# Kernel optimization log

Measured on AMD Instinct MI355X. Metric: run time of the kernel, lower is better.

The kernel has to match this reference:

```python
import jax, jax.numpy as jnp
import numpy as np
import math

N = 50000      # nodes
E = 600000     # edges per relation
R = 3          # relations (graph.etypes)
IN = 256       # in_feats
H = 128        # h_feats
D_ORDER = 2    # Bernstein order d -> d+1 thetas, each of length d+1


def _bernstein_thetas(d):
    # Coefficients (ascending powers) of (x/2)^i (1-x/2)^(d-i) / Beta(i+1, d+1-i)
    thetas = []
    for i in range(d + 1):
        a = np.zeros(i + 1); a[i] = 0.5 ** i                      # (x/2)^i
        b = np.array([math.comb(d - i, j) * (-0.5) ** j for j in range(d - i + 1)])  # (1-x/2)^(d-i)
        scale = math.factorial(d + 1) / (math.factorial(i) * math.factorial(d - i))  # 1/Beta
        thetas.append((np.convolve(a, b) * scale).astype(np.float32))
    return np.stack(thetas)  # [d+1, d+1]

THETAS = jnp.asarray(_bernstein_thetas(D_ORDER))  # [3, 3]


def _leaky(x):
    return jax.nn.leaky_relu(x, 0.01)


def _poly_feats(h, src, dst, n, k):
    # Laplacian power features T_0..T_{k-1}: T_0 = h, T_{j+1} = T_j - Dinv * A^T (Dinv * T_j)
    deg = jax.ops.segment_sum(jnp.ones_like(dst, dtype=h.dtype), dst, num_segments=n)
    dinv = jnp.clip(deg, 1.0) ** -0.5
    dinv = dinv[:, None]  # [N,1]
    feats = [h]
    f = h
    for _ in range(k - 1):
        agg = jax.ops.segment_sum((f * dinv)[src], dst, num_segments=n)  # copy_u + sum
        f = f - agg * dinv
        feats.append(f)
    return jnp.stack(feats)  # [k, N, H]


def setup_inputs() -> dict:
    key = jax.random.key(0)
    ks = jax.random.split(key, 32)
    inp = {"x": jax.random.normal(ks[0], (N, IN), dtype=jnp.float32)}
    for r in range(R):
        inp[f"src{r}"] = jax.random.randint(ks[1 + 2 * r], (E,), 0, N)
        inp[f"dst{r}"] = jax.random.randint(ks[2 + 2 * r], (E,), 0, N)
        inp[f"W1_{r}"] = jax.random.normal(ks[8 + 4 * r], (IN, H), dtype=jnp.float32) * 0.02
        inp[f"b1_{r}"] = jnp.zeros((H,), dtype=jnp.float32)
        inp[f"W2_{r}"] = jax.random.normal(ks[9 + 4 * r], (H, H), dtype=jnp.float32) * 0.02
        inp[f"b2_{r}"] = jnp.zeros((H,), dtype=jnp.float32)
    inp["W3"] = jax.random.normal(ks[30], (H * (D_ORDER + 1), H), dtype=jnp.float32) * 0.02
    inp["b3"] = jnp.zeros((H,), dtype=jnp.float32)
    return inp


def reference(x, src0, dst0, src1, dst1, src2, dst2,
              W1_0, b1_0, W2_0, b2_0,
              W1_1, b1_1, W2_1, b2_1,
              W1_2, b1_2, W2_2, b2_2,
              W3, b3):
    edges = [(src0, dst0), (src1, dst1), (src2, dst2)]
    params = [(W1_0, b1_0, W2_0, b2_0), (W1_1, b1_1, W2_1, b2_1), (W1_2, b1_2, W2_2, b2_2)]
    k = D_ORDER + 1
    acc = jnp.zeros((N, H), dtype=x.dtype)
    for (src, dst), (W1, b1, W2, b2) in zip(edges, params):
        h = _leaky(x @ W1 + b1)
        h = _leaky(h @ W2 + b2)            # dropout is identity in eval
        T = _poly_feats(h, src, dst, N, k)  # [k, N, H]
        # each PolyConv output j: sum_k theta[j,k] * T_k, concatenated over j
        hs = jnp.einsum('jk,knh->jnh', THETAS, T)          # [k, N, H]
        h_final = hs.transpose(1, 0, 2).reshape(N, k * H)   # concat along feature dim
        acc = acc + (h_final @ W3 + b3)
    return _leaky(acc)
```

## Files before the change

kernel.cpp:

```cpp
#include <hip/hip_runtime.h>
#include <hip/hip_bf16.h>

#define HDIM 128
#define TB_LD 1152
#define BCAP 8192
#define NBUCK 256

typedef __attribute__((ext_vector_type(8))) short short8;
typedef __attribute__((ext_vector_type(16))) float floatx16;

#define GF_LEAKY 1
#define GF_BF16  4

__global__ __launch_bounds__(256) void gemm_lds_kernel(
    const __hip_bfloat16* __restrict__ A, int lda, int aOff,
    const __hip_bfloat16* __restrict__ Bt, int ldb, int bRowOff,
    const float* __restrict__ bias, int biasOff,
    void* __restrict__ Cout, int ldc, int cColOff,
    int M, int K, int flags)
{
    __shared__ short As[128 * 64];
    __shared__ short Bs[128 * 64];

    const int tid  = threadIdx.x;
    const int lane = tid & 63;
    const int wave = tid >> 6;
    const int wm   = (wave >> 1) << 6;
    const int wn   = (wave & 1) << 6;
    const int l31  = lane & 31;
    const int ch   = lane >> 5;
    const int e7   = l31 & 7;

    const int m0 = blockIdx.x * 128;
    const int y  = blockIdx.y;

    const short* Ab = (const short*)A + (size_t)y * aOff;
    const short* Bb = (const short*)Bt + (size_t)y * bRowOff * ldb;

    const int rr = tid >> 3;
    const int cc = tid & 7;
    const int sbase = rr * 64 + (((cc ^ (rr & 7)) << 3));
    const short* pA[4];
    const short* pB[4];
#pragma unroll
    for (int i = 0; i < 4; i++) {
        int r = i * 32 + rr;
        int gr = m0 + r; gr = gr < M ? gr : (M - 1);
        pA[i] = Ab + (size_t)gr * lda + cc * 8;
        pB[i] = Bb + (size_t)r * ldb + cc * 8;
    }

    floatx16 acc[2][2];
#pragma unroll
    for (int a = 0; a < 2; a++)
#pragma unroll
        for (int b = 0; b < 2; b++)
#pragma unroll
            for (int i = 0; i < 16; i++) acc[a][b][i] = 0.f;

    const int ra0 = (wm + l31) * 64;
    const int ra1 = (wm + 32 + l31) * 64;
    const int rb0 = (wn + l31) * 64;
    const int rb1 = (wn + 32 + l31) * 64;

    for (int k0 = 0; k0 < K; k0 += 64) {
#pragma unroll
        for (int i = 0; i < 4; i++) {
            int4 av = *(const int4*)(pA[i] + k0);
            int4 bv = *(const int4*)(pB[i] + k0);
            *(int4*)(As + i * 2048 + sbase) = av;
            *(int4*)(Bs + i * 2048 + sbase) = bv;
        }
        __syncthreads();
#pragma unroll
        for (int ks = 0; ks < 4; ks++) {
            const int sw = (((ks << 1) + ch) ^ e7) << 3;
            short8 a0 = *(const short8*)(As + ra0 + sw);
            short8 a1 = *(const short8*)(As + ra1 + sw);
            short8 b0 = *(const short8*)(Bs + rb0 + sw);
            short8 b1 = *(const short8*)(Bs + rb1 + sw);
            acc[0][0] = __builtin_amdgcn_mfma_f32_32x32x16_bf16(a0, b0, acc[0][0], 0, 0, 0);
            acc[0][1] = __builtin_amdgcn_mfma_f32_32x32x16_bf16(a0, b1, acc[0][1], 0, 0, 0);
            acc[1][0] = __builtin_amdgcn_mfma_f32_32x32x16_bf16(a1, b0, acc[1][0], 0, 0, 0);
            acc[1][1] = __builtin_amdgcn_mfma_f32_32x32x16_bf16(a1, b1, acc[1][1], 0, 0, 0);
        }
        __syncthreads();
    }

    const int colL0 = wn + l31;
    const int ccol  = y * cColOff;
    const float bv0 = bias ? bias[y * biasOff + colL0] : 0.f;
    const float bv1 = bias ? bias[y * biasOff + colL0 + 32] : 0.f;
    const int rb = m0 + wm + ((lane >> 5) << 2);

#pragma unroll
    for (int tm = 0; tm < 2; tm++) {
#pragma unroll
        for (int rg = 0; rg < 16; rg++) {
            int row = rb + tm * 32 + (rg & 3) + ((rg >> 2) << 3);
            if (row >= M) continue;
            float v0 = acc[tm][0][rg] + bv0;
            float v1 = acc[tm][1][rg] + bv1;
            if (flags & GF_LEAKY) {
                v0 = v0 > 0.f ? v0 : 0.01f * v0;
                v1 = v1 > 0.f ? v1 : 0.01f * v1;
            }
            if (flags & GF_BF16) {
                __hip_bfloat16* C = (__hip_bfloat16*)Cout;
                C[(size_t)row * ldc + ccol + colL0]      = __float2bfloat16(v0);
                C[(size_t)row * ldc + ccol + colL0 + 32] = __float2bfloat16(v1);
            } else {
                float* C = (float*)Cout;
                C[(size_t)row * ldc + ccol + colL0]      = v0;
                C[(size_t)row * ldc + ccol + colL0 + 32] = v1;
            }
        }
    }
}

__global__ __launch_bounds__(256) void cvt_x_kernel(const float* __restrict__ in,
                                                    __hip_bfloat16* __restrict__ out,
                                                    int n4)
{
    int i = blockIdx.x * 256 + threadIdx.x;
    if (i >= n4) return;
    float4 v = *(const float4*)(in + (size_t)i * 4);
    __hip_bfloat16 o[4] = {__float2bfloat16(v.x), __float2bfloat16(v.y),
                           __float2bfloat16(v.z), __float2bfloat16(v.w)};
    *(uint2*)(out + (size_t)i * 4) = *(uint2*)o;
}

__global__ __launch_bounds__(256) void prep_weights_kernel(
    const float* __restrict__ W1_0, const float* __restrict__ W1_1, const float* __restrict__ W1_2,
    const float* __restrict__ W2_0, const float* __restrict__ W2_1, const float* __restrict__ W2_2,
    const float* __restrict__ W3,
    const float* __restrict__ b1_0, const float* __restrict__ b1_1, const float* __restrict__ b1_2,
    const float* __restrict__ b2_0, const float* __restrict__ b2_1, const float* __restrict__ b2_2,
    __hip_bfloat16* __restrict__ W1t, __hip_bfloat16* __restrict__ W2t,
    __hip_bfloat16* __restrict__ W3et, float* __restrict__ b1c, float* __restrict__ b2c)
{
    int idx = blockIdx.x * 256 + threadIdx.x;
    if (idx < 98304) {
        int r = idx >> 15, rem = idx & 32767;
        int k = rem >> 7, n = rem & 127;
        const float* W = (r == 0) ? W1_0 : (r == 1) ? W1_1 : W1_2;
        W1t[(size_t)(r * 128 + n) * 256 + k] = __float2bfloat16(W[rem]);
    } else if (idx < 147456) {
        int j = idx - 98304;
        int r = j >> 14, rem = j & 16383;
        int k = rem >> 7, n = rem & 127;
        const float* W = (r == 0) ? W2_0 : (r == 1) ? W2_1 : W2_2;
        W2t[(size_t)r * 16384 + n * 128 + k] = __float2bfloat16(W[rem]);
    } else if (idx < 196608) {
        int j = idx - 147456;
        int row = j >> 7, c = j & 127;
        int kk = row >> 7, hh = row & 127;
        const float t[3][3] = {{3.f, -3.f, 0.75f},
                               {0.f,  3.f, -1.5f},
                               {0.f,  0.f, 0.75f}};
        float s = 0.f;
        for (int jj = 0; jj < 3; jj++)
            s += t[jj][kk] * W3[((size_t)jj * HDIM + hh) * HDIM + c];
        __hip_bfloat16 sb = __float2bfloat16(s);
        W3et[(size_t)c * TB_LD + row]       = sb;
        W3et[(size_t)c * TB_LD + 384 + row] = sb;
        W3et[(size_t)c * TB_LD + 768 + row] = sb;
    } else if (idx < 196992) {
        int j = idx - 196608;
        const float* b = (j < 128) ? b1_0 : (j < 256) ? b1_1 : b1_2;
        b1c[j] = b[j & 127];
    } else if (idx < 197376) {
        int j = idx - 196992;
        const float* b = (j < 128) ? b2_0 : (j < 256) ? b2_1 : b2_2;
        b2c[j] = b[j & 127];
    }
}

__global__ __launch_bounds__(256) void bin_kernel(
    const int* __restrict__ s0, const int* __restrict__ s1, const int* __restrict__ s2,
    const int* __restrict__ d0, const int* __restrict__ d1, const int* __restrict__ d2,
    int* __restrict__ bcur,
    int* __restrict__ binned,
    int nE)
{
    __shared__ int hist[NBUCK];
    __shared__ int claim[NBUCK];
    const int t = threadIdx.x;
    const int y = blockIdx.y;
    const int* sp = (y == 0) ? s0 : (y == 1) ? s1 : s2;
    const int* dp = (y == 0) ? d0 : (y == 1) ? d1 : d2;
    const int base = blockIdx.x * 4096;

    hist[t] = 0;
    __syncthreads();

    int pk[16], bk[16], rk[16];
#pragma unroll
    for (int j = 0; j < 16; j++) {
        int e = base + j * 256 + t;
        if (e < nE) {
            int s = sp[e], d = dp[e];
            bk[j] = d >> 8;
            pk[j] = s | ((d & 255) << 16);
            rk[j] = atomicAdd(&hist[bk[j]], 1);
        } else {
            bk[j] = -1;
        }
    }
    __syncthreads();
    int cnt = hist[t];
    claim[t] = (cnt > 0) ? atomicAdd(&bcur[y * NBUCK + t], cnt) : 0;
    __syncthreads();
#pragma unroll
    for (int j = 0; j < 16; j++) {
        if (bk[j] >= 0) {
            int pos = claim[bk[j]] + rk[j];
            if (pos < BCAP)
                binned[((size_t)(y * NBUCK + bk[j])) * BCAP + pos] = pk[j];
        }
    }
}

__global__ __launch_bounds__(256) void deg_kernel2(
    const int* __restrict__ bcur, const int* __restrict__ binned,
    int* __restrict__ degi, float* __restrict__ dinvAll, int N)
{
    __shared__ int hist[256];
    const int t = threadIdx.x;
    const int b = blockIdx.x;
    const int y = blockIdx.y;
    hist[t] = 0;
    __syncthreads();
    const int count = bcur[y * NBUCK + b];
    const int* eb = binned + ((size_t)(y * NBUCK + b)) * BCAP;
    for (int i = t; i < count; i += 256)
        atomicAdd(&hist[(eb[i] >> 16) & 255], 1);
    __syncthreads();
    int node = (b << 8) + t;
    if (node < N) {
        int dg = hist[t];
        degi[(size_t)y * N + node] = dg;
        float d = dg > 1 ? (float)dg : 1.0f;
        dinvAll[(size_t)y * N + node] = 1.0f / sqrtf(d);
    }
}

__global__ __launch_bounds__(256) void place_kernel2(
    const int* __restrict__ bcur, const int* __restrict__ binned,
    const int* __restrict__ rowstart, int* __restrict__ ebuf, int N, int nE)
{
    __shared__ int cur[256];
    const int t = threadIdx.x;
    const int b = blockIdx.x;
    const int y = blockIdx.y;
    int node = (b << 8) + t;
    cur[t] = rowstart[(size_t)y * (N + 1) + (node < N ? node : N)];
    __syncthreads();
    const int count = bcur[y * NBUCK + b];
    const int* eb = binned + ((size_t)(y * NBUCK + b)) * BCAP;
    int* ebo = ebuf + (size_t)y * nE;
    for (int i = t; i < count; i += 256) {
        int p = eb[i];
        int pos = atomicAdd(&cur[(p >> 16) & 255], 1);
        ebo[pos] = p & 0xFFFF;
    }
}

__global__ __launch_bounds__(256) void scan_local_kernel(
    const int* __restrict__ degi, int* __restrict__ rowstart,
    int* __restrict__ bsum, int n)
{
    __shared__ int sdata[256];
    const int y = blockIdx.y;
    const int* in = degi + (size_t)y * n;
    int* out = rowstart + (size_t)y * (n + 1);
    int* bs  = bsum + y * 256;
    const int base = blockIdx.x * 1024;
    const int t = threadIdx.x;
    int v[4];
#pragma unroll
    for (int j = 0; j < 4; j++) {
        int idx = base + t * 4 + j;
        v[j] = (idx < n) ? in[idx] : 0;
    }
    int tsum = v[0] + v[1] + v[2] + v[3];
    sdata[t] = tsum;
    __syncthreads();
    for (int off = 1; off < 256; off <<= 1) {
        int x = (t >= off) ? sdata[t - off] : 0;
        __syncthreads();
        sdata[t] += x;
        __syncthreads();
    }
    int run = sdata[t] - tsum;
    if (t == 255) bs[blockIdx.x] = sdata[255];
#pragma unroll
    for (int j = 0; j < 4; j++) {
        int idx = base + t * 4 + j;
        if (idx < n) out[idx] = run;
        run += v[j];
    }
}

__global__ __launch_bounds__(256) void scan_bsum_kernel(int* __restrict__ bsum, int nB)
{
    __shared__ int sdata[256];
    int* bs = bsum + blockIdx.y * 256;
    const int t = threadIdx.x;
    int val = (t < nB) ? bs[t] : 0;
    sdata[t] = val;
    __syncthreads();
    for (int off = 1; off < 256; off <<= 1) {
        int x = (t >= off) ? sdata[t - off] : 0;
        __syncthreads();
        sdata[t] += x;
        __syncthreads();
    }
    if (t < nB) bs[t] = sdata[t] - val;
}

__global__ __launch_bounds__(256) void scan_add_kernel(
    int* __restrict__ rowstart, const int* __restrict__ bsum, int n, int nE)
{
    int i = blockIdx.x * 256 + threadIdx.x;
    int y = blockIdx.y;
    int* rs = rowstart + (size_t)y * (n + 1);
    const int* bs = bsum + y * 256;
    if (i < n) {
        rs[i] = rs[i] + bs[i >> 10];
    } else if (i == n) {
        rs[n] = nE;
    }
}

__device__ inline float bflo(unsigned u) {
    return __builtin_bit_cast(float, u << 16);
}
__device__ inline float bfhi(unsigned u) {
    return __builtin_bit_cast(float, u & 0xffff0000u);
}

__device__ inline void acc8(float* s, uint4 u, float w) {
    s[0] += bflo(u.x) * w; s[1] += bfhi(u.x) * w;
    s[2] += bflo(u.y) * w; s[3] += bfhi(u.y) * w;
    s[4] += bflo(u.z) * w; s[5] += bfhi(u.z) * w;
    s[6] += bflo(u.w) * w; s[7] += bfhi(u.w) * w;
}

__global__ __launch_bounds__(256) void gather_agg_kernel(
    const int* __restrict__ rowstart, const int* __restrict__ ebufAll,
    const float* __restrict__ dinvAll, __hip_bfloat16* __restrict__ T,
    int inBase, int outBase, int N, int nE)
{
    int v = blockIdx.x * 16 + (threadIdx.x >> 4);
    if (v >= N) return;
    const int y = blockIdx.y;
    const int* rs = rowstart + (size_t)y * (N + 1);
    const int* eb = ebufAll + (size_t)y * nE;
    const float* dinv = dinvAll + (size_t)y * N;
    const int inOff  = y * 384 + inBase;
    const int outOff = y * 384 + outBase;

    const int lane8 = (threadIdx.x & 15) << 3;
    const unsigned short* Tu = (const unsigned short*)T;
    const int beg = rs[v];
    const int end = rs[v + 1];

    float s[8];
#pragma unroll
    for (int j = 0; j < 8; j++) s[j] = 0.f;

    int i = beg;
    for (; i + 3 < end; i += 4) {
        int a = eb[i], b = eb[i + 1], c = eb[i + 2], d = eb[i + 3];
        float wa = dinv[a], wb = dinv[b], wc = dinv[c], wd = dinv[d];
        uint4 ua = *(const uint4*)(Tu + (size_t)a * TB_LD + inOff + lane8);
        uint4 ub = *(const uint4*)(Tu + (size_t)b * TB_LD + inOff + lane8);
        uint4 uc = *(const uint4*)(Tu + (size_t)c * TB_LD + inOff + lane8);
        uint4 ud = *(const uint4*)(Tu + (size_t)d * TB_LD + inOff + lane8);
        acc8(s, ua, wa); acc8(s, ub, wb); acc8(s, uc, wc); acc8(s, ud, wd);
    }
    for (; i < end; i++) {
        int a = eb[i];
        float wa = dinv[a];
        uint4 ua = *(const uint4*)(Tu + (size_t)a * TB_LD + inOff + lane8);
        acc8(s, ua, wa);
    }

    const float di = dinv[v];
    uint4 uv = *(const uint4*)(Tu + (size_t)v * TB_LD + inOff + lane8);
    float r[8] = {bflo(uv.x) - s[0] * di, bfhi(uv.x) - s[1] * di,
                  bflo(uv.y) - s[2] * di, bfhi(uv.y) - s[3] * di,
                  bflo(uv.z) - s[4] * di, bfhi(uv.z) - s[5] * di,
                  bflo(uv.w) - s[6] * di, bfhi(uv.w) - s[7] * di};
    __hip_bfloat16 o[8];
#pragma unroll
    for (int j = 0; j < 8; j++) o[j] = __float2bfloat16(r[j]);
    *(uint4*)(T + (size_t)v * TB_LD + outOff + lane8) = *(uint4*)o;
}

extern "C" void kernel_launch(void* const* d_in, const int* in_sizes, int n_in,
                              void* d_out, int out_size, void* d_ws, size_t ws_size,
                              hipStream_t stream)
{
    const int N = in_sizes[0] / 256;
    const int E = in_sizes[1];
    const int IN = 256;

    const float* x = (const float*)d_in[0];
    const int* srcp[3]; const int* dstp[3];
    const float *W1p[3], *b1p[3], *W2p[3], *b2p[3];
    if (in_sizes[3] == E) {
        for (int r = 0; r < 3; r++) {
            srcp[r] = (const int*)d_in[1 + 2 * r];
            dstp[r] = (const int*)d_in[2 + 2 * r];
            W1p[r]  = (const float*)d_in[7 + 4 * r];
            b1p[r]  = (const float*)d_in[8 + 4 * r];
            W2p[r]  = (const float*)d_in[9 + 4 * r];
            b2p[r]  = (const float*)d_in[10 + 4 * r];
        }
    } else {
        for (int r = 0; r < 3; r++) {
            int base = 1 + 6 * r;
            srcp[r] = (const int*)d_in[base];
            dstp[r] = (const int*)d_in[base + 1];
            W1p[r]  = (const float*)d_in[base + 2];
            b1p[r]  = (const float*)d_in[base + 3];
            W2p[r]  = (const float*)d_in[base + 4];
            b2p[r]  = (const float*)d_in[base + 5];
        }
    }
    const float* W3 = (const float*)d_in[19];
    const float* b3 = (const float*)d_in[20];
    float* out = (float*)d_out;

    char* w = (char*)d_ws;
    auto alloc = [&](size_t bytes) { char* p = w; w += (bytes + 255) & ~(size_t)255; return p; };
    __hip_bfloat16* Tball = (__hip_bfloat16*)alloc((size_t)N * TB_LD * 2);
    __hip_bfloat16* Hb    = (__hip_bfloat16*)alloc((size_t)N * 384 * 2);
    __hip_bfloat16* xb    = (__hip_bfloat16*)alloc((size_t)N * IN * 2);
    __hip_bfloat16* W1t   = (__hip_bfloat16*)alloc((size_t)384 * IN * 2);
    __hip_bfloat16* W2t   = (__hip_bfloat16*)alloc((size_t)3 * HDIM * HDIM * 2);
    __hip_bfloat16* W3et  = (__hip_bfloat16*)alloc((size_t)HDIM * TB_LD * 2);
    float* b1c    = (float*)alloc(384 * 4);
    float* b2c    = (float*)alloc(384 * 4);
    float* dinv   = (float*)alloc((size_t)3 * N * 4);
    int* rowstart = (int*)alloc((size_t)3 * (N + 1) * 4);
    int* degi     = (int*)alloc((size_t)3 * N * 4);
    int* bsum     = (int*)alloc(3 * 256 * 4);
    int* ebuf     = (int*)alloc((size_t)3 * E * 4);
    int* bcur     = (int*)alloc((size_t)3 * NBUCK * 4);
    int* binned   = (int*)alloc((size_t)3 * NBUCK * BCAP * 4);

    const int nB = (N + 1023) / 1024;
    const int mGrid = (N + 127) / 128;
    const int nodeGrid = (N + 15) / 16;
    const int nBuck = (N + 255) >> 8;
    const int binGrid = (E + 4095) / 4096;

    cvt_x_kernel<<<((N * IN / 4) + 255) / 256, 256, 0, stream>>>(x, xb, N * IN / 4);
    prep_weights_kernel<<<(197376 + 255) / 256, 256, 0, stream>>>(
        W1p[0], W1p[1], W1p[2], W2p[0], W2p[1], W2p[2], W3,
        b1p[0], b1p[1], b1p[2], b2p[0], b2p[1], b2p[2],
        W1t, W2t, W3et, b1c, b2c);

    hipMemsetAsync(bcur, 0, (size_t)3 * NBUCK * sizeof(int), stream);
    bin_kernel<<<dim3(binGrid, 3), 256, 0, stream>>>(
        srcp[0], srcp[1], srcp[2], dstp[0], dstp[1], dstp[2], bcur, binned, E);
    deg_kernel2<<<dim3(nBuck, 3), 256, 0, stream>>>(bcur, binned, degi, dinv, N);
    scan_local_kernel<<<dim3(nB, 3), 256, 0, stream>>>(degi, rowstart, bsum, N);
    scan_bsum_kernel<<<dim3(1, 3), 256, 0, stream>>>(bsum, nB);
    scan_add_kernel<<<dim3((N + 256) / 256, 3), 256, 0, stream>>>(rowstart, bsum, N, E);
    place_kernel2<<<dim3(nBuck, 3), 256, 0, stream>>>(bcur, binned, rowstart, ebuf, N, E);

    gemm_lds_kernel<<<dim3(mGrid, 3), 256, 0, stream>>>(
        xb, IN, 0, W1t, IN, 128, b1c, 128, Hb, 384, 128, N, IN,
        GF_LEAKY | GF_BF16);

    gemm_lds_kernel<<<dim3(mGrid, 3), 256, 0, stream>>>(
        Hb, 384, 128, W2t, HDIM, 128, b2c, 128, Tball, TB_LD, 384, N, HDIM,
        GF_LEAKY | GF_BF16);

    gather_agg_kernel<<<dim3(nodeGrid, 3), 256, 0, stream>>>(
        rowstart, ebuf, dinv, Tball, 0, 128, N, E);
    gather_agg_kernel<<<dim3(nodeGrid, 3), 256, 0, stream>>>(
        rowstart, ebuf, dinv, Tball, 128, 256, N, E);

    gemm_lds_kernel<<<dim3(mGrid, 1), 256, 0, stream>>>(
        Tball, TB_LD, 0, W3et, TB_LD, 0, b3, 0, out, HDIM, 0, N, TB_LD,
        GF_LEAKY);
}
```

Before: 420.8 us.

## Fuse x conversion into first GEMM, streamline CSR scan, narrow edge indices

Drops the separate fp32-to-bf16 conversion of x and has the first GEMM load fp32 A tiles and convert them while staging into LDS. The three-kernel degree scan becomes a per-bucket base scan plus an in-block scan inside deg_kernel2, removing two launches and the degree buffer. Edge index storage is cut to 16-bit. The gather kernel is re-split so each node's 128 features are spread over four column blocks of 32, each handled by four threads. In exchange, the first GEMM reads twice the bytes for A, rereading them for each of the three relations, and the gather re-reads edge lists and dinv four times.

Result: slower. 506.7 us (+20.4%).

```diff
diff --git a/kernel.cpp b/kernel.cpp
--- a/kernel.cpp
+++ b/kernel.cpp
@@ -118,16 +118,105 @@
     }
 }
 
-__global__ __launch_bounds__(256) void cvt_x_kernel(const float* __restrict__ in,
-                                                    __hip_bfloat16* __restrict__ out,
-                                                    int n4)
-{
-    int i = blockIdx.x * 256 + threadIdx.x;
-    if (i >= n4) return;
-    float4 v = *(const float4*)(in + (size_t)i * 4);
-    __hip_bfloat16 o[4] = {__float2bfloat16(v.x), __float2bfloat16(v.y),
-                           __float2bfloat16(v.z), __float2bfloat16(v.w)};
-    *(uint2*)(out + (size_t)i * 4) = *(uint2*)o;
+__global__ __launch_bounds__(256) void gemm_lds_a32_kernel(
+    const float* __restrict__ A, int lda,
+    const __hip_bfloat16* __restrict__ Bt, int ldb, int bRowOff,
+    const float* __restrict__ bias, int biasOff,
+    __hip_bfloat16* __restrict__ Cout, int ldc, int cColOff,
+    int M, int K)
+{
+    __shared__ short As[128 * 64];
+    __shared__ short Bs[128 * 64];
+
+    const int tid  = threadIdx.x;
+    const int lane = tid & 63;
+    const int wave = tid >> 6;
+    const int wm   = (wave >> 1) << 6;
+    const int wn   = (wave & 1) << 6;
+    const int l31  = lane & 31;
+    const int ch   = lane >> 5;
+    const int e7   = l31 & 7;
+
+    const int m0 = blockIdx.x * 128;
+    const int y  = blockIdx.y;
+    const short* Bb = (const short*)Bt + (size_t)y * bRowOff * ldb;
+
+    const int rr = tid >> 3;
+    const int cc = tid & 7;
+    const int sbase = rr * 64 + (((cc ^ (rr & 7)) << 3));
+    const float* pA[4];
+    const short* pB[4];
+#pragma unroll
+    for (int i = 0; i < 4; i++) {
+        int r = i * 32 + rr;
+        int gr = m0 + r; gr = gr < M ? gr : (M - 1);
+        pA[i] = A + (size_t)gr * lda + cc * 8;
+        pB[i] = Bb + (size_t)r * ldb + cc * 8;
+    }
+
+    floatx16 acc[2][2];
+#pragma unroll
+    for (int a = 0; a < 2; a++)
+#pragma unroll
+        for (int b = 0; b < 2; b++)
+#pragma unroll
+            for (int i = 0; i < 16; i++) acc[a][b][i] = 0.f;
+
+    const int ra0 = (wm + l31) * 64;
+    const int ra1 = (wm + 32 + l31) * 64;
+    const int rb0 = (wn + l31) * 64;
+    const int rb1 = (wn + 32 + l31) * 64;
+
+    for (int k0 = 0; k0 < K; k0 += 64) {
+#pragma unroll
+        for (int i = 0; i < 4; i++) {
+            float4 a0 = *(const float4*)(pA[i] + k0);
+            float4 a1 = *(const float4*)(pA[i] + k0 + 4);
+            int4 bv = *(const int4*)(pB[i] + k0);
+            __hip_bfloat16 o[8] = {
+                __float2bfloat16(a0.x), __float2bfloat16(a0.y),
+                __float2bfloat16(a0.z), __float2bfloat16(a0.w),
+                __float2bfloat16(a1.x), __float2bfloat16(a1.y),
+                __float2bfloat16(a1.z), __float2bfloat16(a1.w)};
+            *(int4*)(As + i * 2048 + sbase) = *(int4*)o;
+            *(int4*)(Bs + i * 2048 + sbase) = bv;
+        }
+        __syncthreads();
+#pragma unroll
+        for (int ks = 0; ks < 4; ks++) {
+            const int sw = (((ks << 1) + ch) ^ e7) << 3;
+            short8 a0 = *(const short8*)(As + ra0 + sw);
+            short8 a1 = *(const short8*)(As + ra1 + sw);
+            short8 b0 = *(const short8*)(Bs + rb0 + sw);
+            short8 b1 = *(const short8*)(Bs + rb1 + sw);
+            acc[0][0] = __builtin_amdgcn_mfma_f32_32x32x16_bf16(a0, b0, acc[0][0], 0, 0, 0);
+            acc[0][1] = __builtin_amdgcn_mfma_f32_32x32x16_bf16(a0, b1, acc[0][1], 0, 0, 0);
+            acc[1][0] = __builtin_amdgcn_mfma_f32_32x32x16_bf16(a1, b0, acc[1][0], 0, 0, 0);
+            acc[1][1] = __builtin_amdgcn_mfma_f32_32x32x16_bf16(a1, b1, acc[1][1], 0, 0, 0);
+        }
+        __syncthreads();
+    }
+
+    const int colL0 = wn + l31;
+    const int ccol  = y * cColOff;
+    const float bv0 = bias ? bias[y * biasOff + colL0] : 0.f;
+    const float bv1 = bias ? bias[y * biasOff + colL0 + 32] : 0.f;
+    const int rb = m0 + wm + ((lane >> 5) << 2);
+
+#pragma unroll
+    for (int tm = 0; tm < 2; tm++) {
+#pragma unroll
+        for (int rg = 0; rg < 16; rg++) {
+            int row = rb + tm * 32 + (rg & 3) + ((rg >> 2) << 3);
+            if (row >= M) continue;
+            float v0 = acc[tm][0][rg] + bv0;
+            float v1 = acc[tm][1][rg] + bv1;
+            v0 = v0 > 0.f ? v0 : 0.01f * v0;
+            v1 = v1 > 0.f ? v1 : 0.01f * v1;
+            Cout[(size_t)row * ldc + ccol + colL0]      = __float2bfloat16(v0);
+            Cout[(size_t)row * ldc + ccol + colL0 + 32] = __float2bfloat16(v1);
+        }
+    }
 }
 
 __global__ __launch_bounds__(256) void prep_weights_kernel(
@@ -221,11 +310,33 @@
     }
 }
 
+__global__ __launch_bounds__(256) void scan_bcur_kernel(
+    const int* __restrict__ bcur, int* __restrict__ bbase)
+{
+    __shared__ int sdata[256];
+    const int t = threadIdx.x;
+    for (int y = 0; y < 3; y++) {
+        int v = bcur[y * NBUCK + t];
+        sdata[t] = v;
+        __syncthreads();
+        for (int off = 1; off < 256; off <<= 1) {
+            int x = (t >= off) ? sdata[t - off] : 0;
+            __syncthreads();
+            sdata[t] += x;
+            __syncthreads();
+        }
+        bbase[y * NBUCK + t] = sdata[t] - v;
+        __syncthreads();
+    }
+}
+
 __global__ __launch_bounds__(256) void deg_kernel2(
-    const int* __restrict__ bcur, const int* __restrict__ binned,
-    int* __restrict__ degi, float* __restrict__ dinvAll, int N)
+    const int* __restrict__ bcur, const int* __restrict__ bbase,
+    const int* __restrict__ binned,
+    int* __restrict__ rowstart, float* __restrict__ dinvAll, int N)
 {
     __shared__ int hist[256];
+    __shared__ int scanbuf[256];
     const int t = threadIdx.x;
     const int b = blockIdx.x;
     const int y = blockIdx.y;
@@ -236,18 +347,31 @@
     for (int i = t; i < count; i += 256)
         atomicAdd(&hist[(eb[i] >> 16) & 255], 1);
     __syncthreads();
+    int hv = hist[t];
+    scanbuf[t] = hv;
+    __syncthreads();
+    for (int off = 1; off < 256; off <<= 1) {
+        int x = (t >= off) ? scanbuf[t - off] : 0;
+        __syncthreads();
+        scanbuf[t] += x;
+        __syncthreads();
+    }
+    int excl = scanbuf[t] - hv;
     int node = (b << 8) + t;
+    int base = bbase[y * NBUCK + b];
     if (node < N) {
-        int dg = hist[t];
-        degi[(size_t)y * N + node] = dg;
-        float d = dg > 1 ? (float)dg : 1.0f;
+        rowstart[(size_t)y * (N + 1) + node] = base + excl;
+        float d = hv > 1 ? (float)hv : 1.0f;
         dinvAll[(size_t)y * N + node] = 1.0f / sqrtf(d);
+    } else if (node == N) {
+        rowstart[(size_t)y * (N + 1) + node] = base + excl;
     }
 }
 
 __global__ __launch_bounds__(256) void place_kernel2(
     const int* __restrict__ bcur, const int* __restrict__ binned,
-    const int* __restrict__ rowstart, int* __restrict__ ebuf, int N, int nE)
+    const int* __restrict__ rowstart, unsigned short* __restrict__ ebuf,
+    int N, int nE)
 {
     __shared__ int cur[256];
     const int t = threadIdx.x;
@@ -258,78 +382,11 @@
     __syncthreads();
     const int count = bcur[y * NBUCK + b];
     const int* eb = binned + ((size_t)(y * NBUCK + b)) * BCAP;
-    int* ebo = ebuf + (size_t)y * nE;
+    unsigned short* ebo = ebuf + (size_t)y * nE;
     for (int i = t; i < count; i += 256) {
         int p = eb[i];
         int pos = atomicAdd(&cur[(p >> 16) & 255], 1);
-        ebo[pos] = p & 0xFFFF;
-    }
-}
-
-__global__ __launch_bounds__(256) void scan_local_kernel(
-    const int* __restrict__ degi, int* __restrict__ rowstart,
-    int* __restrict__ bsum, int n)
-{
-    __shared__ int sdata[256];
-    const int y = blockIdx.y;
-    const int* in = degi + (size_t)y * n;
-    int* out = rowstart + (size_t)y * (n + 1);
-    int* bs  = bsum + y * 256;
-    const int base = blockIdx.x * 1024;
-    const int t = threadIdx.x;
-    int v[4];
-#pragma unroll
-    for (int j = 0; j < 4; j++) {
-        int idx = base + t * 4 + j;
-        v[j] = (idx < n) ? in[idx] : 0;
-    }
-    int tsum = v[0] + v[1] + v[2] + v[3];
-    sdata[t] = tsum;
-    __syncthreads();
-    for (int off = 1; off < 256; off <<= 1) {
-        int x = (t >= off) ? sdata[t - off] : 0;
-        __syncthreads();
-        sdata[t] += x;
-        __syncthreads();
-    }
-    int run = sdata[t] - tsum;
-    if (t == 255) bs[blockIdx.x] = sdata[255];
-#pragma unroll
-    for (int j = 0; j < 4; j++) {
-        int idx = base + t * 4 + j;
-        if (idx < n) out[idx] = run;
-        run += v[j];
-    }
-}
-
-__global__ __launch_bounds__(256) void scan_bsum_kernel(int* __restrict__ bsum, int nB)
-{
-    __shared__ int sdata[256];
-    int* bs = bsum + blockIdx.y * 256;
-    const int t = threadIdx.x;
-    int val = (t < nB) ? bs[t] : 0;
-    sdata[t] = val;
-    __syncthreads();
-    for (int off = 1; off < 256; off <<= 1) {
-        int x = (t >= off) ? sdata[t - off] : 0;
-        __syncthreads();
-        sdata[t] += x;
-        __syncthreads();
-    }
-    if (t < nB) bs[t] = sdata[t] - val;
-}
-
-__global__ __launch_bounds__(256) void scan_add_kernel(
-    int* __restrict__ rowstart, const int* __restrict__ bsum, int n, int nE)
-{
-    int i = blockIdx.x * 256 + threadIdx.x;
-    int y = blockIdx.y;
-    int* rs = rowstart + (size_t)y * (n + 1);
-    const int* bs = bsum + y * 256;
-    if (i < n) {
-        rs[i] = rs[i] + bs[i >> 10];
-    } else if (i == n) {
-        rs[n] = nE;
+        ebo[pos] = (unsigned short)(p & 0xFFFF);
     }
 }
 
@@ -348,20 +405,21 @@
 }
 
 __global__ __launch_bounds__(256) void gather_agg_kernel(
-    const int* __restrict__ rowstart, const int* __restrict__ ebufAll,
+    const int* __restrict__ rowstart, const unsigned short* __restrict__ ebufAll,
     const float* __restrict__ dinvAll, __hip_bfloat16* __restrict__ T,
     int inBase, int outBase, int N, int nE)
 {
-    int v = blockIdx.x * 16 + (threadIdx.x >> 4);
+    const int v = blockIdx.x * 64 + (threadIdx.x >> 2);
     if (v >= N) return;
-    const int y = blockIdx.y;
-    const int* rs = rowstart + (size_t)y * (N + 1);
-    const int* eb = ebufAll + (size_t)y * nE;
-    const float* dinv = dinvAll + (size_t)y * N;
-    const int inOff  = y * 384 + inBase;
-    const int outOff = y * 384 + outBase;
-
-    const int lane8 = (threadIdx.x & 15) << 3;
+    const int y   = blockIdx.y;
+    const int rel = y >> 2;
+    const int cb  = y & 3;
+    const int* rs = rowstart + (size_t)rel * (N + 1);
+    const unsigned short* eb = ebufAll + (size_t)rel * nE;
+    const float* dinv = dinvAll + (size_t)rel * N;
+    const int inOff  = rel * 384 + inBase  + cb * 32 + (threadIdx.x & 3) * 8;
+    const int outOff = rel * 384 + outBase + cb * 32 + (threadIdx.x & 3) * 8;
+
     const unsigned short* Tu = (const unsigned short*)T;
     const int beg = rs[v];
     const int end = rs[v + 1];
@@ -374,21 +432,21 @@
     for (; i + 3 < end; i += 4) {
         int a = eb[i], b = eb[i + 1], c = eb[i + 2], d = eb[i + 3];
         float wa = dinv[a], wb = dinv[b], wc = dinv[c], wd = dinv[d];
-        uint4 ua = *(const uint4*)(Tu + (size_t)a * TB_LD + inOff + lane8);
-        uint4 ub = *(const uint4*)(Tu + (size_t)b * TB_LD + inOff + lane8);
-        uint4 uc = *(const uint4*)(Tu + (size_t)c * TB_LD + inOff + lane8);
-        uint4 ud = *(const uint4*)(Tu + (size_t)d * TB_LD + inOff + lane8);
+        uint4 ua = *(const uint4*)(Tu + (size_t)a * TB_LD + inOff);
+        uint4 ub = *(const uint4*)(Tu + (size_t)b * TB_LD + inOff);
+        uint4 uc = *(const uint4*)(Tu + (size_t)c * TB_LD + inOff);
+        uint4 ud = *(const uint4*)(Tu + (size_t)d * TB_LD + inOff);
         acc8(s, ua, wa); acc8(s, ub, wb); acc8(s, uc, wc); acc8(s, ud, wd);
     }
     for (; i < end; i++) {
         int a = eb[i];
         float wa = dinv[a];
-        uint4 ua = *(const uint4*)(Tu + (size_t)a * TB_LD + inOff + lane8);
+        uint4 ua = *(const uint4*)(Tu + (size_t)a * TB_LD + inOff);
         acc8(s, ua, wa);
     }
 
     const float di = dinv[v];
-    uint4 uv = *(const uint4*)(Tu + (size_t)v * TB_LD + inOff + lane8);
+    uint4 uv = *(const uint4*)(Tu + (size_t)v * TB_LD + inOff);
     float r[8] = {bflo(uv.x) - s[0] * di, bfhi(uv.x) - s[1] * di,
                   bflo(uv.y) - s[2] * di, bfhi(uv.y) - s[3] * di,
                   bflo(uv.z) - s[4] * di, bfhi(uv.z) - s[5] * di,
@@ -396,7 +454,7 @@
     __hip_bfloat16 o[8];
 #pragma unroll
     for (int j = 0; j < 8; j++) o[j] = __float2bfloat16(r[j]);
-    *(uint4*)(T + (size_t)v * TB_LD + outOff + lane8) = *(uint4*)o;
+    *(uint4*)(T + (size_t)v * TB_LD + outOff) = *(uint4*)o;
 }
 
 extern "C" void kernel_launch(void* const* d_in, const int* in_sizes, int n_in,
@@ -438,7 +496,6 @@
     auto alloc = [&](size_t bytes) { char* p = w; w += (bytes + 255) & ~(size_t)255; return p; };
     __hip_bfloat16* Tball = (__hip_bfloat16*)alloc((size_t)N * TB_LD * 2);
     __hip_bfloat16* Hb    = (__hip_bfloat16*)alloc((size_t)N * 384 * 2);
-    __hip_bfloat16* xb    = (__hip_bfloat16*)alloc((size_t)N * IN * 2);
     __hip_bfloat16* W1t   = (__hip_bfloat16*)alloc((size_t)384 * IN * 2);
     __hip_bfloat16* W2t   = (__hip_bfloat16*)alloc((size_t)3 * HDIM * HDIM * 2);
     __hip_bfloat16* W3et  = (__hip_bfloat16*)alloc((size_t)HDIM * TB_LD * 2);
@@ -446,19 +503,16 @@
     float* b2c    = (float*)alloc(384 * 4);
     float* dinv   = (float*)alloc((size_t)3 * N * 4);
     int* rowstart = (int*)alloc((size_t)3 * (N + 1) * 4);
-    int* degi     = (int*)alloc((size_t)3 * N * 4);
-    int* bsum     = (int*)alloc(3 * 256 * 4);
-    int* ebuf     = (int*)alloc((size_t)3 * E * 4);
     int* bcur     = (int*)alloc((size_t)3 * NBUCK * 4);
+    int* bbase    = (int*)alloc((size_t)3 * NBUCK * 4);
+    unsigned short* ebuf = (unsigned short*)alloc((size_t)3 * E * 2);
     int* binned   = (int*)alloc((size_t)3 * NBUCK * BCAP * 4);
 
-    const int nB = (N + 1023) / 1024;
     const int mGrid = (N + 127) / 128;
-    const int nodeGrid = (N + 15) / 16;
     const int nBuck = (N + 255) >> 8;
     const int binGrid = (E + 4095) / 4096;
-
-    cvt_x_kernel<<<((N * IN / 4) + 255) / 256, 256, 0, stream>>>(x, xb, N * IN / 4);
+    const int gGrid = (N + 63) / 64;
+
     prep_weights_kernel<<<(197376 + 255) / 256, 256, 0, stream>>>(
         W1p[0], W1p[1], W1p[2], W2p[0], W2p[1], W2p[2], W3,
         b1p[0], b1p[1], b1p[2], b2p[0], b2p[1], b2p[2],
@@ -467,23 +521,22 @@
     hipMemsetAsync(bcur, 0, (size_t)3 * NBUCK * sizeof(int), stream);
     bin_kernel<<<dim3(binGrid, 3), 256, 0, stream>>>(
         srcp[0], srcp[1], srcp[2], dstp[0], dstp[1], dstp[2], bcur, binned, E);
-    deg_kernel2<<<dim3(nBuck, 3), 256, 0, stream>>>(bcur, binned, degi, dinv, N);
-    scan_local_kernel<<<dim3(nB, 3), 256, 0, stream>>>(degi, rowstart, bsum, N);
-    scan_bsum_kernel<<<dim3(1, 3), 256, 0, stream>>>(bsum, nB);
-    scan_add_kernel<<<dim3((N + 256) / 256, 3), 256, 0, stream>>>(rowstart, bsum, N, E);
-    place_kernel2<<<dim3(nBuck, 3), 256, 0, stream>>>(bcur, binned, rowstart, ebuf, N, E);
-
-    gemm_lds_kernel<<<dim3(mGrid, 3), 256, 0, stream>>>(
-        xb, IN, 0, W1t, IN, 128, b1c, 128, Hb, 384, 128, N, IN,
-        GF_LEAKY | GF_BF16);
+    scan_bcur_kernel<<<1, 256, 0, stream>>>(bcur, bbase);
+    deg_kernel2<<<dim3(nBuck, 3), 256, 0, stream>>>(bcur, bbase, binned,
+                                                    rowstart, dinv, N);
+    place_kernel2<<<dim3(nBuck, 3), 256, 0, stream>>>(bcur, binned, rowstart,
+                                                      ebuf, N, E);
+
+    gemm_lds_a32_kernel<<<dim3(mGrid, 3), 256, 0, stream>>>(
+        x, IN, W1t, IN, 128, b1c, 128, Hb, 384, 128, N, IN);
 
     gemm_lds_kernel<<<dim3(mGrid, 3), 256, 0, stream>>>(
         Hb, 384, 128, W2t, HDIM, 128, b2c, 128, Tball, TB_LD, 384, N, HDIM,
         GF_LEAKY | GF_BF16);
 
-    gather_agg_kernel<<<dim3(nodeGrid, 3), 256, 0, stream>>>(
+    gather_agg_kernel<<<dim3(gGrid, 12), 256, 0, stream>>>(
         rowstart, ebuf, dinv, Tball, 0, 128, N, E);
-    gather_agg_kernel<<<dim3(nodeGrid, 3), 256, 0, stream>>>(
+    gather_agg_kernel<<<dim3(gGrid, 12), 256, 0, stream>>>(
         rowstart, ebuf, dinv, Tball, 128, 256, N, E);
 
     gemm_lds_kernel<<<dim3(mGrid, 1), 256, 0, stream>>>(
```
